# Kernel optimization log

Hardware: AMD Instinct MI355X
Metric: run time of the kernel (lower is better)

The kernel has to match this reference:

```python
import jax, jax.numpy as jnp
import numpy as np

B, T, C = 4, 2048, 1024
H = 16
D = C // H  # head_dim = 64


def setup_inputs() -> dict:
    key = jax.random.key(0)
    k1, k2, k3 = jax.random.split(key, 3)
    x = jax.random.normal(k1, (B, T, C), dtype=jnp.float32)
    w_qkv = jax.random.normal(k2, (C, 3 * C), dtype=jnp.float32) * (C ** -0.5)
    b_qkv = jnp.zeros((3 * C,), dtype=jnp.float32)
    w_proj = jax.random.normal(k3, (C, C), dtype=jnp.float32) * (C ** -0.5)
    b_proj = jnp.zeros((C,), dtype=jnp.float32)
    return {"x": x, "w_qkv": w_qkv, "b_qkv": b_qkv, "w_proj": w_proj, "b_proj": b_proj}


def reference(x, w_qkv, b_qkv, w_proj, b_proj):
    # qkv projection: (B,T,C) -> (B,T,3,H,D) -> q,k,v each (B,H,T,D)
    qkv = (x @ w_qkv + b_qkv).reshape(B, T, 3, H, D)
    q, k, v = jnp.moveaxis(qkv, 2, 0)           # each (B, T, H, D)
    q = q.transpose(0, 2, 1, 3)                 # (B, H, T, D)
    k = k.transpose(0, 2, 1, 3)
    v = v.transpose(0, 2, 1, 3)

    scale = 1.0 / jnp.sqrt(jnp.float32(D))
    attn = jnp.einsum('bhqd,bhkd->bhqk', q, k) * scale  # (B,H,T,T)
    causal = jnp.tril(jnp.ones((T, T), dtype=bool))
    attn = jnp.where(causal[None, None], attn, -jnp.inf)
    attn = jax.nn.softmax(attn, axis=-1)
    # dropout p=0.0 (eval mode) -> identity
    out = jnp.einsum('bhqk,bhkd->bhqd', attn, v)        # (B,H,T,D)
    out = out.transpose(0, 2, 1, 3).reshape(B, T, C)
    return out @ w_proj + b_proj
```

## Files before the change

kernel.cpp:

```cpp
#include <hip/hip_runtime.h>
#include <hip/hip_bf16.h>


#define Bsz 4
#define Tsz 2048
#define Csz 1024
#define Hn  16
#define Dh  64

typedef unsigned short u16;
typedef __attribute__((ext_vector_type(8))) short bf16x8;
typedef __attribute__((ext_vector_type(4))) float f32x4;
typedef __attribute__((ext_vector_type(4))) unsigned int u32x4;
typedef __attribute__((ext_vector_type(2))) unsigned int u32x2;

__device__ __forceinline__ u16 f2b(float f) {
  __hip_bfloat16 h = __float2bfloat16(f);
  return *reinterpret_cast<u16*>(&h);
}

__device__ __forceinline__ unsigned pk2(float lo, float hi) {
  return (unsigned)f2b(lo) | ((unsigned)f2b(hi) << 16);
}

__device__ __forceinline__ void gld_lds16(const void* g, void* lds) {
  __builtin_amdgcn_global_load_lds(
      (const __attribute__((address_space(1))) unsigned int*)g,
      (__attribute__((address_space(3))) unsigned int*)lds, 16, 0, 0);
}

__global__ __launch_bounds__(256) void cvt_f32_bf16(const float* __restrict__ in,
                                                    u16* __restrict__ out) {
  size_t i = ((size_t)blockIdx.x * 256 + threadIdx.x) * 8;
  f32x4 a = *(const f32x4*)(in + i);
  f32x4 b = *(const f32x4*)(in + i + 4);
  u16 r[8];
#pragma unroll
  for (int j = 0; j < 4; ++j) { r[j] = f2b(a[j]); r[4 + j] = f2b(b[j]); }
  *(u32x4*)(out + i) = *(const u32x4*)r;
}

__global__ __launch_bounds__(256) void cvt_transpose(const float* __restrict__ in,
                                                     u16* __restrict__ out,
                                                     int R, int C) {
  __shared__ u16 tile[64 * 66];
  const int r0 = blockIdx.x * 64, c0 = blockIdx.y * 64;
  const int tid = threadIdx.x;
#pragma unroll
  for (int i = 0; i < 16; ++i) {
    int idx = i * 256 + tid;
    int r = idx >> 6, c = idx & 63;
    tile[r * 66 + c] = f2b(in[(size_t)(r0 + r) * C + (c0 + c)]);
  }
  __syncthreads();
#pragma unroll
  for (int i = 0; i < 16; ++i) {
    int idx = i * 256 + tid;
    int c = idx >> 6, r = idx & 63;
    out[(size_t)(c0 + c) * R + (r0 + r)] = tile[r * 66 + c];
  }
}

__device__ __forceinline__ void gemm_tile_acc(const u16* __restrict__ A,
                                              const u16* __restrict__ Bt,
                                              int m0, int n0,
                                              u16* Alds, u16* Blds,
                                              f32x4 acc[4][4]) {
  const int tid = threadIdx.x;
  const int w = tid >> 6, lane = tid & 63;
  const int wm = w & 1, wn = w >> 1;
  const int col = lane & 15, quad = lane >> 4;
  const int lrow = lane >> 2;
  const int kseg = (lane & 3) * 8;
#pragma unroll
  for (int mt = 0; mt < 4; ++mt)
#pragma unroll
    for (int nt = 0; nt < 4; ++nt)
      acc[mt][nt] = (f32x4){0.f, 0.f, 0.f, 0.f};

  for (int k0 = 0; k0 < 1024; k0 += 32) {
    __syncthreads();
#pragma unroll
    for (int g = 0; g < 2; ++g) {
      int grp = w * 2 + g;
      gld_lds16(A + (size_t)(m0 + grp * 16 + lrow) * 1024 + k0 + kseg,
                (char*)Alds + grp * 1024);
      gld_lds16(Bt + (size_t)(n0 + grp * 16 + lrow) * 1024 + k0 + kseg,
                (char*)Blds + grp * 1024);
    }
    __syncthreads();
    bf16x8 af[4], bfr[4];
#pragma unroll
    for (int mt = 0; mt < 4; ++mt)
      af[mt] = *(const bf16x8*)(Alds + (wm * 64 + mt * 16 + col) * 32 + quad * 8);
#pragma unroll
    for (int nt = 0; nt < 4; ++nt)
      bfr[nt] = *(const bf16x8*)(Blds + (wn * 64 + nt * 16 + col) * 32 + quad * 8);
#pragma unroll
    for (int mt = 0; mt < 4; ++mt)
#pragma unroll
      for (int nt = 0; nt < 4; ++nt)
        acc[mt][nt] = __builtin_amdgcn_mfma_f32_16x16x32_bf16(af[mt], bfr[nt],
                                                              acc[mt][nt], 0, 0, 0);
  }
}

__global__ __launch_bounds__(256) void gemm_qkv(const u16* __restrict__ X,
                                                const u16* __restrict__ WT,
                                                const float* __restrict__ bias,
                                                u16* __restrict__ Q,
                                                u16* __restrict__ Kc,
                                                u16* __restrict__ Vt) {
  __shared__ __align__(16) u16 Alds[128 * 32];
  __shared__ __align__(16) u16 Blds[128 * 32];
  f32x4 acc[4][4];
  const int m0 = blockIdx.x * 128, n0 = blockIdx.y * 128;
  gemm_tile_acc(X, WT, m0, n0, Alds, Blds, acc);

  const float qscale = 0.18033688011112042f;
  const int tid = threadIdx.x;
  const int w = tid >> 6, lane = tid & 63;
  const int wm = w & 1, wn = w >> 1;
  const int col = lane & 15, quad = lane >> 4;
#pragma unroll
  for (int mt = 0; mt < 4; ++mt)
#pragma unroll
    for (int nt = 0; nt < 4; ++nt) {
      int n = n0 + wn * 64 + nt * 16 + col;
      int s = n >> 10, hh = (n >> 6) & (Hn - 1), d = n & 63;
      int mBase = m0 + wm * 64 + mt * 16 + quad * 4;
      int b = mBase >> 11, t0 = mBase & (Tsz - 1);
      if (s == 2) {
        u16 vals[4];
#pragma unroll
        for (int r = 0; r < 4; ++r) vals[r] = f2b(acc[mt][nt][r] + bias[n]);
        *(u32x2*)(Vt + ((size_t)(b * Hn + hh) * Dh + d) * Tsz + t0) =
            *(const u32x2*)vals;
      } else {
        const float scl = (s == 0) ? qscale : 1.f;
        u16* dst = (s == 0) ? Q : Kc;
#pragma unroll
        for (int r = 0; r < 4; ++r)
          dst[((size_t)(b * Hn + hh) * Tsz + (t0 + r)) * Dh + d] =
              f2b((acc[mt][nt][r] + bias[n]) * scl);
      }
    }
}

__global__ __launch_bounds__(256) void gemm_proj(const u16* __restrict__ O,
                                                 const u16* __restrict__ WT,
                                                 const float* __restrict__ bias,
                                                 float* __restrict__ out) {
  __shared__ __align__(16) u16 Alds[128 * 32];
  __shared__ __align__(16) u16 Blds[128 * 32];
  f32x4 acc[4][4];
  const int m0 = blockIdx.x * 128, n0 = blockIdx.y * 128;
  gemm_tile_acc(O, WT, m0, n0, Alds, Blds, acc);

  const int tid = threadIdx.x;
  const int w = tid >> 6, lane = tid & 63;
  const int wm = w & 1, wn = w >> 1;
  const int col = lane & 15, quad = lane >> 4;
#pragma unroll
  for (int mt = 0; mt < 4; ++mt)
#pragma unroll
    for (int nt = 0; nt < 4; ++nt)
#pragma unroll
      for (int r = 0; r < 4; ++r) {
        int m = m0 + wm * 64 + mt * 16 + quad * 4 + r;
        int n = n0 + wn * 64 + nt * 16 + col;
        out[(size_t)m * Csz + n] = acc[mt][nt][r] + bias[n];
      }
}

__global__ __launch_bounds__(256, 3) void attn(const u16* __restrict__ Q,
                                               const u16* __restrict__ Kg,
                                               const u16* __restrict__ Vt,
                                               u16* __restrict__ O) {
  __shared__ __align__(16) u16 Ks[3][64 * 64];
  __shared__ __align__(16) u16 Vs[3][64 * 64];

  const int d0 = blockIdx.x + (blockIdx.y << 5) + (blockIdx.z << 9);
  const int xcd = d0 & 7, rest = d0 >> 3;
  const int j = rest & 31, ghi = rest >> 5;
  const int bh = (ghi << 3) + xcd;
  const int qt = 31 - j;
  const int h = bh & (Hn - 1), b = bh >> 4;

  const int tid = threadIdx.x, w = tid >> 6, lane = tid & 63;
  const int col = lane & 15, quad = lane >> 4;
  const int qbase = qt * 64;

  const u16* Kbase = Kg + (size_t)bh * Tsz * Dh;
  const u16* Vbase = Vt + (size_t)bh * Dh * Tsz;

  const u16* Qg = Q + ((size_t)bh * Tsz + qbase) * Dh;
  bf16x8 aq[2];
#pragma unroll
  for (int ks = 0; ks < 2; ++ks)
    aq[ks] = *(const bf16x8*)(Qg + (size_t)(w * 16 + col) * Dh + ks * 32 + quad * 8);
  asm volatile("s_waitcnt vmcnt(0)" ::: "memory");

  const int xseg = ((tid & 7) ^ ((tid >> 3) & 7)) * 8;
  const size_t koff = (size_t)(tid >> 3) * 64 + xseg;
  const size_t voff = (size_t)(tid >> 3) * Tsz + xseg;
  const int swz = col & 7;
  const int off0 = ((0 + quad) ^ swz) << 3;
  const int off1 = ((4 + quad) ^ swz) << 3;

  f32x4 oacc[4];
#pragma unroll
  for (int dt = 0; dt < 4; ++dt) oacc[dt] = (f32x4){0.f, 0.f, 0.f, 0.f};
  float lsum[4] = {0.f, 0.f, 0.f, 0.f};

  const int nst = qt + 1;
  gld_lds16(Kbase + koff, &Ks[0][w * 512]);
  gld_lds16(Kbase + 2048 + koff, &Ks[0][2048 + w * 512]);
  gld_lds16(Vbase + voff, &Vs[0][w * 512]);
  gld_lds16(Vbase + (size_t)32 * Tsz + voff, &Vs[0][2048 + w * 512]);
  if (1 < nst) {
    gld_lds16(Kbase + 4096 + koff, &Ks[1][w * 512]);
    gld_lds16(Kbase + 4096 + 2048 + koff, &Ks[1][2048 + w * 512]);
    gld_lds16(Vbase + 64 + voff, &Vs[1][w * 512]);
    gld_lds16(Vbase + 64 + (size_t)32 * Tsz + voff, &Vs[1][2048 + w * 512]);
  }
  const u16* kdma = Kbase + 2 * 4096 + koff;
  const u16* vdma = Vbase + 2 * 64 + voff;

  int cur = 0;
  for (int s = 0; s < nst; ++s) {
    if (s + 1 < nst) {
      asm volatile("s_waitcnt vmcnt(4)" ::: "memory");
    } else {
      asm volatile("s_waitcnt vmcnt(0)" ::: "memory");
    }
    __builtin_amdgcn_s_barrier();
    __builtin_amdgcn_sched_barrier(0);
    if (s + 2 < nst) {
      int pf = cur + 2; if (pf >= 3) pf -= 3;
      gld_lds16(kdma, &Ks[pf][w * 512]);
      gld_lds16(kdma + 2048, &Ks[pf][2048 + w * 512]);
      gld_lds16(vdma, &Vs[pf][w * 512]);
      gld_lds16(vdma + (size_t)32 * Tsz, &Vs[pf][2048 + w * 512]);
      kdma += 4096;
      vdma += 64;
    }

    f32x4 sacc[4];
#pragma unroll
    for (int kt = 0; kt < 4; ++kt) sacc[kt] = (f32x4){0.f, 0.f, 0.f, 0.f};
#pragma unroll
    for (int ks = 0; ks < 2; ++ks)
#pragma unroll
      for (int kt = 0; kt < 4; ++kt) {
        bf16x8 bk = *(const bf16x8*)(
            &Ks[cur][(kt * 16 + col) * 64 + (ks ? off1 : off0)]);
        sacc[kt] = __builtin_amdgcn_mfma_f32_16x16x32_bf16(bk, aq[ks],
                                                           sacc[kt], 0, 0, 0);
      }

    float e[4][4];
    if (s == qt) {
      const int qg = w * 16 + col;
#pragma unroll
      for (int kt = 0; kt < 4; ++kt)
#pragma unroll
        for (int r = 0; r < 4; ++r) {
          int kl = kt * 16 + quad * 4 + r;
          float p = (kl > qg) ? 0.f : exp2f(sacc[kt][r]);
          lsum[kt] += p;
          e[kt][r] = p;
        }
    } else {
#pragma unroll
      for (int kt = 0; kt < 4; ++kt)
#pragma unroll
        for (int r = 0; r < 4; ++r) {
          float p = exp2f(sacc[kt][r]);
          lsum[kt] += p;
          e[kt][r] = p;
        }
    }

#pragma unroll
    for (int ksg = 0; ksg < 2; ++ksg) {
      unsigned w00 = pk2(e[2 * ksg][0], e[2 * ksg][1]);
      unsigned w01 = pk2(e[2 * ksg][2], e[2 * ksg][3]);
      unsigned w10 = pk2(e[2 * ksg + 1][0], e[2 * ksg + 1][1]);
      unsigned w11 = pk2(e[2 * ksg + 1][2], e[2 * ksg + 1][3]);
      auto ra = __builtin_amdgcn_permlane32_swap(w00, w10, false, false);
      auto rb = __builtin_amdgcn_permlane32_swap(w01, w11, false, false);
      auto sa = __builtin_amdgcn_permlane16_swap(ra[0], ra[1], false, false);
      auto sb = __builtin_amdgcn_permlane16_swap(rb[0], rb[1], false, false);
      union { unsigned u[4]; bf16x8 v; } pf;
      pf.u[0] = sa[0]; pf.u[1] = sb[0]; pf.u[2] = sa[1]; pf.u[3] = sb[1];
#pragma unroll
      for (int dt = 0; dt < 4; ++dt) {
        bf16x8 bv = *(const bf16x8*)(
            &Vs[cur][(dt * 16 + col) * 64 + (ksg ? off1 : off0)]);
        oacc[dt] = __builtin_amdgcn_mfma_f32_16x16x32_bf16(bv, pf.v,
                                                           oacc[dt], 0, 0, 0);
      }
    }

    cur += 1; if (cur >= 3) cur = 0;
  }

  float v = (lsum[0] + lsum[1]) + (lsum[2] + lsum[3]);
  v += __shfl_xor(v, 16);
  v += __shfl_xor(v, 32);
  const float inv = 1.0f / v;

  const int rg = qbase + w * 16 + col;
  u16* Orow = O + (((size_t)b * Tsz + rg) * Hn + h) * Dh;
#pragma unroll
  for (int dt = 0; dt < 4; ++dt) {
    u16 vals[4];
#pragma unroll
    for (int r = 0; r < 4; ++r) vals[r] = f2b(oacc[dt][r] * inv);
    *(u32x2*)(Orow + dt * 16 + quad * 4) = *(const u32x2*)vals;
  }
}

extern "C" void kernel_launch(void* const* d_in, const int* in_sizes, int n_in,
                              void* d_out, int out_size, void* d_ws, size_t ws_size,
                              hipStream_t stream) {
  const float* x      = (const float*)d_in[0];
  const float* w_qkv  = (const float*)d_in[1];
  const float* b_qkv  = (const float*)d_in[2];
  const float* w_proj = (const float*)d_in[3];
  const float* b_proj = (const float*)d_in[4];
  float* out = (float*)d_out;

  u16* Xb     = (u16*)d_ws;
  u16* WqkvT  = Xb + (size_t)8192 * 1024;
  u16* WprojT = WqkvT + (size_t)3072 * 1024;
  u16* Qb     = WprojT + (size_t)1024 * 1024;
  u16* Kb     = Qb + (size_t)8192 * 1024;
  u16* Ob     = Kb + (size_t)8192 * 1024;
  u16* Vtb    = (u16*)d_out;

  cvt_f32_bf16<<<4096, 256, 0, stream>>>(x, Xb);
  cvt_transpose<<<dim3(16, 48), 256, 0, stream>>>(w_qkv, WqkvT, 1024, 3072);
  cvt_transpose<<<dim3(16, 16), 256, 0, stream>>>(w_proj, WprojT, 1024, 1024);
  gemm_qkv<<<dim3(64, 24), 256, 0, stream>>>(Xb, WqkvT, b_qkv, Qb, Kb, Vtb);
  attn<<<dim3(32, 16, 4), 256, 0, stream>>>(Qb, Kb, Vtb, Ob);
  gemm_proj<<<dim3(64, 8), 256, 0, stream>>>(Ob, WprojT, b_proj, out);
}
```

Before: 273.6 us.

## Use 128-row query tiles with 8 waves and double-buffered KV in attention

Each attention block now covers 128 query rows with 512 threads (8 waves), so every K/V tile loaded into LDS is reused by twice as many query rows. The triple buffer becomes a double buffer, and each step waits for vmcnt(0) before its barrier. The grid-to-(batch,head,qtile) mapping is rebuilt to pair short and long causal tiles and keep heads grouped by XCD. The lower waves skip the final fully masked KV tile. This halves K/V global traffic per query but exposes more load latency, because prefetch depth drops from two tiles to one.

```diff
diff --git a/kernel.cpp b/kernel.cpp
--- a/kernel.cpp
+++ b/kernel.cpp
@@ -173,26 +173,40 @@
       }
 }
 
-__global__ __launch_bounds__(256, 3) void attn(const u16* __restrict__ Q,
+__global__ __launch_bounds__(512, 6) void attn(const u16* __restrict__ Q,
                                                const u16* __restrict__ Kg,
                                                const u16* __restrict__ Vt,
                                                u16* __restrict__ O) {
-  __shared__ __align__(16) u16 Ks[3][64 * 64];
-  __shared__ __align__(16) u16 Vs[3][64 * 64];
-
-  const int d0 = blockIdx.x + (blockIdx.y << 5) + (blockIdx.z << 9);
-  const int xcd = d0 & 7, rest = d0 >> 3;
-  const int j = rest & 31, ghi = rest >> 5;
-  const int bh = (ghi << 3) + xcd;
-  const int qt = 31 - j;
+  __shared__ __align__(16) u16 Ks[2][64 * 64];
+  __shared__ __align__(16) u16 Vs[2][64 * 64];
+
+  const int d0 = blockIdx.x + (blockIdx.y << 4) + (blockIdx.z << 8);
+  const int xcd = d0 & 7;
+  const int l = d0 >> 3;
+  const int r0_ = l >> 5, c0_ = l & 31;
+  const int a_ = c0_ >> 1, p_ = c0_ & 1;
+  const int qt = (r0_ & 1) ? a_ : (15 - a_);
+  const int bh = (((p_ << 2) | r0_) << 3) | xcd;
   const int h = bh & (Hn - 1), b = bh >> 4;
 
   const int tid = threadIdx.x, w = tid >> 6, lane = tid & 63;
   const int col = lane & 15, quad = lane >> 4;
-  const int qbase = qt * 64;
+  const int qbase = qt << 7;
 
   const u16* Kbase = Kg + (size_t)bh * Tsz * Dh;
   const u16* Vbase = Vt + (size_t)bh * Dh * Tsz;
+
+  const int trow = tid >> 3;
+  const int xseg = ((tid & 7) ^ (trow & 7)) * 8;
+  const size_t koff = (size_t)trow * 64 + xseg;
+  const size_t voff = (size_t)trow * Tsz + xseg;
+  const int swz = col & 7;
+  const int off0 = ((0 + quad) ^ swz) << 3;
+  const int off1 = ((4 + quad) ^ swz) << 3;
+
+  const int nst = 2 * qt + 2;
+  gld_lds16(Kbase + koff, &Ks[0][w * 512]);
+  gld_lds16(Vbase + voff, &Vs[0][w * 512]);
 
   const u16* Qg = Q + ((size_t)bh * Tsz + qbase) * Dh;
   bf16x8 aq[2];
@@ -201,109 +215,88 @@
     aq[ks] = *(const bf16x8*)(Qg + (size_t)(w * 16 + col) * Dh + ks * 32 + quad * 8);
   asm volatile("s_waitcnt vmcnt(0)" ::: "memory");
 
-  const int xseg = ((tid & 7) ^ ((tid >> 3) & 7)) * 8;
-  const size_t koff = (size_t)(tid >> 3) * 64 + xseg;
-  const size_t voff = (size_t)(tid >> 3) * Tsz + xseg;
-  const int swz = col & 7;
-  const int off0 = ((0 + quad) ^ swz) << 3;
-  const int off1 = ((4 + quad) ^ swz) << 3;
-
   f32x4 oacc[4];
 #pragma unroll
   for (int dt = 0; dt < 4; ++dt) oacc[dt] = (f32x4){0.f, 0.f, 0.f, 0.f};
   float lsum[4] = {0.f, 0.f, 0.f, 0.f};
 
-  const int nst = qt + 1;
-  gld_lds16(Kbase + koff, &Ks[0][w * 512]);
-  gld_lds16(Kbase + 2048 + koff, &Ks[0][2048 + w * 512]);
-  gld_lds16(Vbase + voff, &Vs[0][w * 512]);
-  gld_lds16(Vbase + (size_t)32 * Tsz + voff, &Vs[0][2048 + w * 512]);
-  if (1 < nst) {
-    gld_lds16(Kbase + 4096 + koff, &Ks[1][w * 512]);
-    gld_lds16(Kbase + 4096 + 2048 + koff, &Ks[1][2048 + w * 512]);
-    gld_lds16(Vbase + 64 + voff, &Vs[1][w * 512]);
-    gld_lds16(Vbase + 64 + (size_t)32 * Tsz + voff, &Vs[1][2048 + w * 512]);
-  }
-  const u16* kdma = Kbase + 2 * 4096 + koff;
-  const u16* vdma = Vbase + 2 * 64 + voff;
-
-  int cur = 0;
+  const u16* kdma = Kbase + 4096 + koff;
+  const u16* vdma = Vbase + 64 + voff;
+
+  const int qg = w * 16 + col;
+  const int smask = 2 * qt + (w >= 4 ? 1 : 0);
+
   for (int s = 0; s < nst; ++s) {
-    if (s + 1 < nst) {
-      asm volatile("s_waitcnt vmcnt(4)" ::: "memory");
-    } else {
-      asm volatile("s_waitcnt vmcnt(0)" ::: "memory");
-    }
+    asm volatile("s_waitcnt vmcnt(0)" ::: "memory");
     __builtin_amdgcn_s_barrier();
     __builtin_amdgcn_sched_barrier(0);
-    if (s + 2 < nst) {
-      int pf = cur + 2; if (pf >= 3) pf -= 3;
-      gld_lds16(kdma, &Ks[pf][w * 512]);
-      gld_lds16(kdma + 2048, &Ks[pf][2048 + w * 512]);
-      gld_lds16(vdma, &Vs[pf][w * 512]);
-      gld_lds16(vdma + (size_t)32 * Tsz, &Vs[pf][2048 + w * 512]);
+    const int cur = s & 1;
+    if (s + 1 < nst) {
+      const int nxt = cur ^ 1;
+      gld_lds16(kdma, &Ks[nxt][w * 512]);
+      gld_lds16(vdma, &Vs[nxt][w * 512]);
       kdma += 4096;
       vdma += 64;
     }
 
-    f32x4 sacc[4];
-#pragma unroll
-    for (int kt = 0; kt < 4; ++kt) sacc[kt] = (f32x4){0.f, 0.f, 0.f, 0.f};
-#pragma unroll
-    for (int ks = 0; ks < 2; ++ks)
-#pragma unroll
-      for (int kt = 0; kt < 4; ++kt) {
-        bf16x8 bk = *(const bf16x8*)(
-            &Ks[cur][(kt * 16 + col) * 64 + (ks ? off1 : off0)]);
-        sacc[kt] = __builtin_amdgcn_mfma_f32_16x16x32_bf16(bk, aq[ks],
-                                                           sacc[kt], 0, 0, 0);
+    if (w >= 4 || s < nst - 1) {
+      f32x4 sacc[4];
+#pragma unroll
+      for (int kt = 0; kt < 4; ++kt) sacc[kt] = (f32x4){0.f, 0.f, 0.f, 0.f};
+#pragma unroll
+      for (int ks = 0; ks < 2; ++ks)
+#pragma unroll
+        for (int kt = 0; kt < 4; ++kt) {
+          bf16x8 bk = *(const bf16x8*)(
+              &Ks[cur][(kt * 16 + col) * 64 + (ks ? off1 : off0)]);
+          sacc[kt] = __builtin_amdgcn_mfma_f32_16x16x32_bf16(bk, aq[ks],
+                                                             sacc[kt], 0, 0, 0);
+        }
+
+      float e[4][4];
+      if (s >= smask) {
+        const int rel = (s - 2 * qt) << 6;
+#pragma unroll
+        for (int kt = 0; kt < 4; ++kt)
+#pragma unroll
+          for (int r = 0; r < 4; ++r) {
+            int kl = rel + kt * 16 + quad * 4 + r;
+            float p = (kl > qg) ? 0.f : exp2f(sacc[kt][r]);
+            lsum[kt] += p;
+            e[kt][r] = p;
+          }
+      } else {
+#pragma unroll
+        for (int kt = 0; kt < 4; ++kt)
+#pragma unroll
+          for (int r = 0; r < 4; ++r) {
+            float p = exp2f(sacc[kt][r]);
+            lsum[kt] += p;
+            e[kt][r] = p;
+          }
       }
 
-    float e[4][4];
-    if (s == qt) {
-      const int qg = w * 16 + col;
-#pragma unroll
-      for (int kt = 0; kt < 4; ++kt)
-#pragma unroll
-        for (int r = 0; r < 4; ++r) {
-          int kl = kt * 16 + quad * 4 + r;
-          float p = (kl > qg) ? 0.f : exp2f(sacc[kt][r]);
-          lsum[kt] += p;
-          e[kt][r] = p;
+#pragma unroll
+      for (int ksg = 0; ksg < 2; ++ksg) {
+        unsigned w00 = pk2(e[2 * ksg][0], e[2 * ksg][1]);
+        unsigned w01 = pk2(e[2 * ksg][2], e[2 * ksg][3]);
+        unsigned w10 = pk2(e[2 * ksg + 1][0], e[2 * ksg + 1][1]);
+        unsigned w11 = pk2(e[2 * ksg + 1][2], e[2 * ksg + 1][3]);
+        auto ra = __builtin_amdgcn_permlane32_swap(w00, w10, false, false);
+        auto rb = __builtin_amdgcn_permlane32_swap(w01, w11, false, false);
+        auto sa = __builtin_amdgcn_permlane16_swap(ra[0], ra[1], false, false);
+        auto sb = __builtin_amdgcn_permlane16_swap(rb[0], rb[1], false, false);
+        union { unsigned u[4]; bf16x8 v; } pf;
+        pf.u[0] = sa[0]; pf.u[1] = sb[0]; pf.u[2] = sa[1]; pf.u[3] = sb[1];
+#pragma unroll
+        for (int dt = 0; dt < 4; ++dt) {
+          bf16x8 bv = *(const bf16x8*)(
+              &Vs[cur][(dt * 16 + col) * 64 + (ksg ? off1 : off0)]);
+          oacc[dt] = __builtin_amdgcn_mfma_f32_16x16x32_bf16(bv, pf.v,
+                                                             oacc[dt], 0, 0, 0);
         }
-    } else {
-#pragma unroll
-      for (int kt = 0; kt < 4; ++kt)
-#pragma unroll
-        for (int r = 0; r < 4; ++r) {
-          float p = exp2f(sacc[kt][r]);
-          lsum[kt] += p;
-          e[kt][r] = p;
-        }
-    }
-
-#pragma unroll
-    for (int ksg = 0; ksg < 2; ++ksg) {
-      unsigned w00 = pk2(e[2 * ksg][0], e[2 * ksg][1]);
-      unsigned w01 = pk2(e[2 * ksg][2], e[2 * ksg][3]);
-      unsigned w10 = pk2(e[2 * ksg + 1][0], e[2 * ksg + 1][1]);
-      unsigned w11 = pk2(e[2 * ksg + 1][2], e[2 * ksg + 1][3]);
-      auto ra = __builtin_amdgcn_permlane32_swap(w00, w10, false, false);
-      auto rb = __builtin_amdgcn_permlane32_swap(w01, w11, false, false);
-      auto sa = __builtin_amdgcn_permlane16_swap(ra[0], ra[1], false, false);
-      auto sb = __builtin_amdgcn_permlane16_swap(rb[0], rb[1], false, false);
-      union { unsigned u[4]; bf16x8 v; } pf;
-      pf.u[0] = sa[0]; pf.u[1] = sb[0]; pf.u[2] = sa[1]; pf.u[3] = sb[1];
-#pragma unroll
-      for (int dt = 0; dt < 4; ++dt) {
-        bf16x8 bv = *(const bf16x8*)(
-            &Vs[cur][(dt * 16 + col) * 64 + (ksg ? off1 : off0)]);
-        oacc[dt] = __builtin_amdgcn_mfma_f32_16x16x32_bf16(bv, pf.v,
-                                                           oacc[dt], 0, 0, 0);
       }
     }
-
-    cur += 1; if (cur >= 3) cur = 0;
   }
 
   float v = (lsum[0] + lsum[1]) + (lsum[2] + lsum[3]);
@@ -344,6 +337,6 @@
   cvt_transpose<<<dim3(16, 48), 256, 0, stream>>>(w_qkv, WqkvT, 1024, 3072);
   cvt_transpose<<<dim3(16, 16), 256, 0, stream>>>(w_proj, WprojT, 1024, 1024);
   gemm_qkv<<<dim3(64, 24), 256, 0, stream>>>(Xb, WqkvT, b_qkv, Qb, Kb, Vtb);
-  attn<<<dim3(32, 16, 4), 256, 0, stream>>>(Qb, Kb, Vtb, Ob);
+  attn<<<dim3(16, 16, 4), 512, 0, stream>>>(Qb, Kb, Vtb, Ob);
   gemm_proj<<<dim3(64, 8), 256, 0, stream>>>(Ob, WprojT, b_proj, out);
 }
```

After: 274.3 us. No clear change (+0.3%).
